# Kernel tuning notes

Measured on AMD Instinct MI355X. Metric: run time of the kernel, lower is better.

## Reference

```python
import jax, jax.numpy as jnp
import numpy as np

HALF = 24576          # per-side HalfKP features (64 king sq * 6 piece * 64 sq)
NUMEL = 2 * HALF      # util.half_kp_numel()
BASE = 128
B = 8192


def _linear(x, W, b):
    return x @ W.T + b


def setup_inputs() -> dict:
    key = jax.random.key(0)
    ks = jax.random.split(key, 16)
    s = 0.01
    return {
        "pov": jax.random.uniform(ks[0], (B, 1), dtype=jnp.float32),
        "white": jax.random.uniform(ks[1], (B, HALF), dtype=jnp.float32),
        "black": jax.random.uniform(ks[2], (B, HALF), dtype=jnp.float32),
        "w_aff_W": jax.random.normal(ks[3], (BASE, NUMEL), dtype=jnp.float32) * s,
        "w_aff_b": jax.random.normal(ks[4], (BASE,), dtype=jnp.float32) * s,
        "b_aff_W": jax.random.normal(ks[5], (BASE, NUMEL), dtype=jnp.float32) * s,
        "b_aff_b": jax.random.normal(ks[6], (BASE,), dtype=jnp.float32) * s,
        "fc0_W": jax.random.normal(ks[7], (32, 2 * BASE), dtype=jnp.float32) * s,
        "fc0_b": jax.random.normal(ks[8], (32,), dtype=jnp.float32) * s,
        "fc1_W": jax.random.normal(ks[9], (32, 32), dtype=jnp.float32) * s,
        "fc1_b": jax.random.normal(ks[10], (32,), dtype=jnp.float32) * s,
        "fc2_W": jax.random.normal(ks[11], (32, 64), dtype=jnp.float32) * s,
        "fc2_b": jax.random.normal(ks[12], (32,), dtype=jnp.float32) * s,
        "fc3_W": jax.random.normal(ks[13], (1, 96), dtype=jnp.float32) * s,
        "fc3_b": jax.random.normal(ks[14], (1,), dtype=jnp.float32) * s,
    }


def reference(pov, white, black, w_aff_W, w_aff_b, b_aff_W, b_aff_b,
              fc0_W, fc0_b, fc1_W, fc1_b, fc2_W, fc2_b, fc3_W, fc3_b):
    # util.half_kp(a, b) = cat([a, b], dim=1)
    w_feat = jnp.concatenate([white, black], axis=1)  # [B, NUMEL]
    b_feat = jnp.concatenate([black, white], axis=1)
    w_ = _linear(w_feat, w_aff_W, w_aff_b)            # [B, 128]
    b_ = _linear(b_feat, b_aff_W, b_aff_b)
    wb = jnp.concatenate([w_, b_], axis=1)            # [B, 256]
    bw = jnp.concatenate([b_, w_], axis=1)
    base = jax.nn.relu(pov * wb + (1.0 - pov) * bw)
    x = jax.nn.relu(_linear(base, fc0_W, fc0_b))      # [B, 32]
    x = jnp.concatenate([x, jax.nn.relu(_linear(x, fc1_W, fc1_b))], axis=1)  # [B, 64]
    x = jnp.concatenate([x, jax.nn.relu(_linear(x, fc2_W, fc2_b))], axis=1)  # [B, 96]
    return _linear(x, fc3_W, fc3_b)                   # [B, 1]
```

## Files before the change

### kernel.cpp

```cpp
#include <hip/hip_runtime.h>
#include <hip/hip_bf16.h>
#include <stdint.h>

typedef float f32x4 __attribute__((ext_vector_type(4)));
typedef float fvec4 __attribute__((ext_vector_type(4)));
typedef short bf16x8 __attribute__((ext_vector_type(8)));

#define HALF_K 24576
#define NUMELK 49152
#define BATCH  8192
#define BM 256
#define BN 256
#define BK 64

#define VMCNT_I(n) asm volatile("s_waitcnt vmcnt(" #n ")" ::: "memory")
#define VMCNT(n) VMCNT_I(n)
#define SCHEDB   __builtin_amdgcn_sched_barrier(0)
#define SBAR     __builtin_amdgcn_s_barrier()

__device__ __forceinline__ short f2bf(float f) {
  __hip_bfloat16 h = __float2bfloat16(f);
  return __builtin_bit_cast(short, h);
}

__device__ __forceinline__ void gload_lds16(const short* g, short* l) {
  __builtin_amdgcn_global_load_lds(
      (const __attribute__((address_space(1))) unsigned*)g,
      (__attribute__((address_space(3))) unsigned*)l, 16, 0, 0);
}

__global__ __launch_bounds__(256)
void nnue_prep(const float* __restrict__ wW, const float* __restrict__ bW,
               short* __restrict__ Bprep) {
  int gid = blockIdx.x * 256 + threadIdx.x;
  int KT  = gid >> 11;
  int rem = gid & 2047;
  int col = rem >> 3;
  int kc  = rem & 7;
  int kg  = KT * 64 + kc * 8;
  const float* src;
  if (col < 128) {
    src = wW + (size_t)col * NUMELK + kg;
  } else {
    int kk = (kg < HALF_K) ? (kg + HALF_K) : (kg - HALF_K);
    src = bW + (size_t)(col - 128) * NUMELK + kk;
  }
  fvec4 v0 = ((const fvec4*)src)[0];
  fvec4 v1 = ((const fvec4*)src)[1];
  bf16x8 o;
  o[0] = f2bf(v0[0]); o[1] = f2bf(v0[1]); o[2] = f2bf(v0[2]); o[3] = f2bf(v0[3]);
  o[4] = f2bf(v1[0]); o[5] = f2bf(v1[1]); o[6] = f2bf(v1[2]); o[7] = f2bf(v1[3]);
  *(bf16x8*)(Bprep + (size_t)KT * 16384 + col * 64 + ((kc ^ (col & 7)) << 3)) = o;
}

__global__ __launch_bounds__(512, 2)
void nnue_gemm(const float* __restrict__ white, const float* __restrict__ black,
               const short* __restrict__ Bprep, float* __restrict__ partial,
               int kchunk, int S) {
  __shared__ short B0s[BN * BK];
  __shared__ short B1s[BN * BK];

  const int t    = threadIdx.x;
  const int lane = t & 63;
  const int w    = t >> 6;

  const int bid = blockIdx.x;
  const int xcd = bid & 7, bi = bid >> 3;
  const int xpk = 8 / S;
  const int ks  = xcd / xpk;
  const int mt  = (xcd % xpk) * (32 / xpk) + bi;
  const int m0  = mt * BM;
  const int k0  = ks * kchunk;
  const int KT0 = k0 / BK;

  f32x4 acc[2][16];
  const f32x4 zero = {0.f, 0.f, 0.f, 0.f};
#pragma unroll
  for (int a = 0; a < 2; ++a)
#pragma unroll
    for (int b = 0; b < 16; ++b) acc[a][b] = zero;

  const int l15 = lane & 15, l4 = lane >> 4;

  const size_t arow_off = (size_t)(m0 + w * 32 + l15) * HALF_K + l4 * 8;

  auto issueA = [&](fvec4* va, int kg) {
    const float* Af; int ka;
    if (kg < HALF_K) { Af = white; ka = kg; } else { Af = black; ka = kg - HALF_K; }
    const float* base = Af + arow_off + ka;
#pragma unroll
    for (int mf = 0; mf < 2; ++mf)
#pragma unroll
      for (int s = 0; s < 2; ++s) {
        const fvec4* p = (const fvec4*)(base + (size_t)mf * 16 * HALF_K + s * 32);
        va[mf * 4 + s * 2]     = p[0];
        va[mf * 4 + s * 2 + 1] = p[1];
      }
  };

  auto issueB = [&](short* dst, int KT) {
    const short* src = Bprep + (size_t)KT * 16384 + w * 2048 + lane * 8;
    short* d = dst + w * 2048;
#pragma unroll
    for (int j = 0; j < 4; ++j)
      gload_lds16(src + j * 512, d + j * 512);
  };

  auto compute = [&](const short* Bb, const fvec4* va) {
#pragma unroll
    for (int s = 0; s < 2; ++s) {
      bf16x8 af[2];
#pragma unroll
      for (int mf = 0; mf < 2; ++mf) {
        const fvec4 lo = va[mf * 4 + s * 2];
        const fvec4 hi = va[mf * 4 + s * 2 + 1];
        af[mf][0] = f2bf(lo[0]); af[mf][1] = f2bf(lo[1]);
        af[mf][2] = f2bf(lo[2]); af[mf][3] = f2bf(lo[3]);
        af[mf][4] = f2bf(hi[0]); af[mf][5] = f2bf(hi[1]);
        af[mf][6] = f2bf(hi[2]); af[mf][7] = f2bf(hi[3]);
      }
      const int kc = s * 4 + l4;
#pragma unroll
      for (int nf = 0; nf < 16; ++nf) {
        int col = nf * 16 + l15;
        bf16x8 bf = *(const bf16x8*)&Bb[col * 64 + ((kc ^ (col & 7)) << 3)];
        acc[0][nf] = __builtin_amdgcn_mfma_f32_16x16x32_bf16(af[0], bf, acc[0][nf], 0, 0, 0);
        acc[1][nf] = __builtin_amdgcn_mfma_f32_16x16x32_bf16(af[1], bf, acc[1][nf], 0, 0, 0);
      }
    }
  };

  const int niter = kchunk / BK;

  fvec4 vaA[8], vaB[8];

  issueB(B0s, KT0);
  issueA(vaA, k0);
  VMCNT(8); SCHEDB;
  SBAR; SCHEDB;

  for (int i = 0; i < niter; i += 2) {
    if (i + 1 < niter) {
      issueB(B1s, KT0 + i + 1);
      issueA(vaB, k0 + (i + 1) * BK);
    }
    SCHEDB;
    compute(B0s, vaA);
    VMCNT(8); SCHEDB;
    SBAR; SCHEDB;

    if (i + 1 < niter) {
      if (i + 2 < niter) {
        issueB(B0s, KT0 + i + 2);
        issueA(vaA, k0 + (i + 2) * BK);
      }
      SCHEDB;
      compute(B1s, vaB);
      VMCNT(8); SCHEDB;
      SBAR; SCHEDB;
    }
  }

  float* P = partial + ((size_t)ks * BATCH + m0) * 256;
#pragma unroll
  for (int mf = 0; mf < 2; ++mf) {
    int row = w * 32 + mf * 16 + l4 * 4;
#pragma unroll
    for (int nf = 0; nf < 16; ++nf) {
      int col = nf * 16 + l15;
#pragma unroll
      for (int rr = 0; rr < 4; ++rr)
        P[(size_t)(row + rr) * 256 + col] = acc[mf][nf][rr];
    }
  }
}

__global__ __launch_bounds__(256)
void nnue_tail(const float* __restrict__ partial, int S,
               const float* __restrict__ pov,
               const float* __restrict__ waffb, const float* __restrict__ baffb,
               const float* __restrict__ fc0W, const float* __restrict__ fc0b,
               const float* __restrict__ fc1W, const float* __restrict__ fc1b,
               const float* __restrict__ fc2W, const float* __restrict__ fc2b,
               const float* __restrict__ fc3W, const float* __restrict__ fc3b,
               float* __restrict__ out) {
  __shared__ float w0s[32 * 256];
  __shared__ float w1s[32 * 32];
  __shared__ float w2s[32 * 64];
  __shared__ float w3s[96];
  __shared__ float b0s[32], b1s[32], b2s[32];
  __shared__ float base_s[4][256];
  __shared__ float b3s;

  const int t = threadIdx.x;
  for (int i = t; i < 8192; i += 256) { int j = i >> 8, k = i & 255; w0s[(j << 8) | ((k + j) & 255)] = fc0W[i]; }
  for (int i = t; i < 1024; i += 256) { int j = i >> 5, k = i & 31;  w1s[(j << 5) | ((k + j) & 31)]  = fc1W[i]; }
  for (int i = t; i < 2048; i += 256) { int j = i >> 6, k = i & 63;  w2s[(j << 6) | ((k + j) & 63)]  = fc2W[i]; }
  if (t < 96) w3s[t] = fc3W[t];
  if (t < 32) { b0s[t] = fc0b[t]; b1s[t] = fc1b[t]; b2s[t] = fc2b[t]; }
  if (t == 0) b3s = fc3b[0];
  __syncthreads();

  const int wid = t >> 6, lane = t & 63;
  const int m = blockIdx.x * 4 + wid;
  const float pv = pov[m];

  float val[4];
  {
    const float* p = partial + (size_t)m * 256 + lane * 4;
    fvec4 a = *(const fvec4*)p;
    for (int s = 1; s < S; ++s) a += *(const fvec4*)(p + (size_t)s * BATCH * 256);
    const int c0 = lane * 4;
#pragma unroll
    for (int j = 0; j < 4; ++j) {
      int c = c0 + j;
      float bias = (c < 128) ? waffb[c] : baffb[c - 128];
      val[j] = a[j] + bias;
    }
  }
#pragma unroll
  for (int j = 0; j < 4; ++j) {
    float other = __shfl(val[j], lane ^ 32, 64);
    if (lane < 32) {
      int c = lane * 4 + j;
      float w = val[j], b = other;
      base_s[wid][c]       = fmaxf(pv * w + (1.f - pv) * b, 0.f);
      base_s[wid][c + 128] = fmaxf(pv * b + (1.f - pv) * w, 0.f);
    }
  }
  __syncthreads();

  const int j = lane & 31, half = lane >> 5;
  const float* bs = &base_s[wid][0];

  float s0 = 0.f;
  for (int k = 0; k < 128; ++k) {
    int kk = half * 128 + k;
    s0 += bs[kk] * w0s[(j << 8) | ((kk + j) & 255)];
  }
  s0 += __shfl(s0, lane ^ 32, 64);
  float x0 = fmaxf(s0 + b0s[j], 0.f);

  float s1 = 0.f;
  for (int k = 0; k < 32; ++k)
    s1 += __shfl(x0, k, 64) * w1s[(j << 5) | ((k + j) & 31)];
  float x1 = fmaxf(s1 + b1s[j], 0.f);

  float s2 = 0.f;
  for (int k = 0; k < 32; ++k) {
    s2 += __shfl(x0, k, 64) * w2s[(j << 6) | ((k + j) & 63)];
    s2 += __shfl(x1, k, 64) * w2s[(j << 6) | ((k + 32 + j) & 63)];
  }
  float x2 = fmaxf(s2 + b2s[j], 0.f);

  float s3 = 0.f;
  for (int k = 0; k < 32; ++k) {
    s3 += __shfl(x0, k, 64) * w3s[k];
    s3 += __shfl(x1, k, 64) * w3s[32 + k];
    s3 += __shfl(x2, k, 64) * w3s[64 + k];
  }
  if (lane == 0) out[m] = s3 + b3s;
}

extern "C" void kernel_launch(void* const* d_in, const int* in_sizes, int n_in,
                              void* d_out, int out_size, void* d_ws, size_t ws_size,
                              hipStream_t stream) {
  const float* pov   = (const float*)d_in[0];
  const float* white = (const float*)d_in[1];
  const float* black = (const float*)d_in[2];
  const float* wW    = (const float*)d_in[3];
  const float* wb    = (const float*)d_in[4];
  const float* bW    = (const float*)d_in[5];
  const float* bb    = (const float*)d_in[6];
  const float* fc0W  = (const float*)d_in[7];
  const float* fc0b  = (const float*)d_in[8];
  const float* fc1W  = (const float*)d_in[9];
  const float* fc1b  = (const float*)d_in[10];
  const float* fc2W  = (const float*)d_in[11];
  const float* fc2b  = (const float*)d_in[12];
  const float* fc3W  = (const float*)d_in[13];
  const float* fc3b  = (const float*)d_in[14];
  float* out = (float*)d_out;

  short* Bprep = (short*)d_ws;
  const size_t BWS_BYTES = (size_t)256 * NUMELK * 2;
  float* partial = (float*)((char*)d_ws + BWS_BYTES);
  const size_t PART1 = (size_t)BATCH * 256 * 4;

  int S = 8;
  if (ws_size < BWS_BYTES + 8 * PART1) S = 4;
  if (ws_size < BWS_BYTES + 4 * PART1) S = 2;
  if (ws_size < BWS_BYTES + 2 * PART1) S = 1;

  nnue_prep<<<dim3(6144), 256, 0, stream>>>(wW, bW, Bprep);
  nnue_gemm<<<dim3(32 * S), 512, 0, stream>>>(white, black, Bprep, partial, NUMELK / S, S);
  nnue_tail<<<dim3(BATCH / 4), 256, 0, stream>>>(partial, S, pov, wb, bb,
      fc0W, fc0b, fc1W, fc1b, fc2W, fc2b, fc3W, fc3b, out);
}
```

Before: 442.7 us.

## Deepen A-register prefetch to two tiles ahead with triple-buffered registers

Replaces the double-buffered A register prefetch with a three-deep rotation, so global loads of A for tile n+2 are issued while tile n is computed and B is loaded into LDS for tile n+1. The loop is unrolled by six with a specialized tail that drains outstanding loads. This aims to hide more global-memory latency on the fp32 activation stream, at the cost of more VGPRs (a third 8x float4 buffer), which could lower occupancy or cause spills. It also assumes niter is a multiple of six and at least six.

Result: slower. 627.3 us (+41.7%).

```diff
diff --git a/kernel.cpp b/kernel.cpp
--- a/kernel.cpp
+++ b/kernel.cpp
@@ -132,33 +132,45 @@
 
   const int niter = kchunk / BK;
 
-  fvec4 vaA[8], vaB[8];
+  fvec4 va0[8], va1[8], va2[8];
+
+  auto iterStep = [&](fvec4* vac, fvec4* van, const short* Bc, short* Bn,
+                      int n, int mode) {
+    if (mode == 0) {
+      issueB(Bn, KT0 + n + 1);
+      issueA(van, k0 + (n + 2) * BK);
+    } else if (mode == 1) {
+      issueB(Bn, KT0 + n + 1);
+    }
+    SCHEDB;
+    compute(Bc, vac);
+    if (mode == 0) { VMCNT(8); SCHEDB; SBAR; SCHEDB; }
+    else if (mode == 1) { VMCNT(0); SCHEDB; SBAR; SCHEDB; }
+  };
 
   issueB(B0s, KT0);
-  issueA(vaA, k0);
-  VMCNT(8); SCHEDB;
-  SBAR; SCHEDB;
-
-  for (int i = 0; i < niter; i += 2) {
-    if (i + 1 < niter) {
-      issueB(B1s, KT0 + i + 1);
-      issueA(vaB, k0 + (i + 1) * BK);
-    }
-    SCHEDB;
-    compute(B0s, vaA);
-    VMCNT(8); SCHEDB;
-    SBAR; SCHEDB;
-
-    if (i + 1 < niter) {
-      if (i + 2 < niter) {
-        issueB(B0s, KT0 + i + 2);
-        issueA(vaA, k0 + (i + 2) * BK);
-      }
-      SCHEDB;
-      compute(B1s, vaB);
-      VMCNT(8); SCHEDB;
-      SBAR; SCHEDB;
-    }
+  issueA(va0, k0);
+  issueA(va1, k0 + BK);
+  VMCNT(8);
+  SCHEDB; SBAR; SCHEDB;
+
+  for (int g = 0; g < niter / 6 - 1; ++g) {
+    const int n = g * 6;
+    iterStep(va0, va2, B0s, B1s, n,     0);
+    iterStep(va1, va0, B1s, B0s, n + 1, 0);
+    iterStep(va2, va1, B0s, B1s, n + 2, 0);
+    iterStep(va0, va2, B1s, B0s, n + 3, 0);
+    iterStep(va1, va0, B0s, B1s, n + 4, 0);
+    iterStep(va2, va1, B1s, B0s, n + 5, 0);
+  }
+  {
+    const int n = niter - 6;
+    iterStep(va0, va2, B0s, B1s, n,     0);
+    iterStep(va1, va0, B1s, B0s, n + 1, 0);
+    iterStep(va2, va1, B0s, B1s, n + 2, 0);
+    iterStep(va0, va2, B1s, B0s, n + 3, 0);
+    iterStep(va1, va0, B0s, B1s, n + 4, 1);
+    iterStep(va2, va1, B1s, B0s, n + 5, 2);
   }
 
   float* P = partial + ((size_t)ks * BATCH + m0) * 256;
```
